# Performance work log

Measured on AMD Instinct MI355X. Metric: run time of the kernel, lower is better.

The kernel has to match this reference:

```python
import jax, jax.numpy as jnp
import numpy as np

HID, INTER, DK = 768, 1536, 128
NEG_INF = 1.0e12
LOG512 = float(np.log(512.0))


def setup_inputs() -> dict:
    key = jax.random.key(0)
    k1, k2, k3 = jax.random.split(key, 3)
    B, S = 4, 2048
    hidden_states = jax.random.normal(k1, (B, S, HID), dtype=jnp.float32)
    attention_mask = jnp.ones((B, S), dtype=jnp.int32)
    # i_dense: hidden -> 2*INTER + DK (no bias); o_dense: INTER -> hidden (no bias)
    Wi = jax.random.normal(k2, (HID, 2 * INTER + DK), dtype=jnp.float32) * (HID ** -0.5)
    Wo = jax.random.normal(k3, (INTER, HID), dtype=jnp.float32) * (INTER ** -0.5)
    q_gamma = jnp.ones((DK,), dtype=jnp.float32)  # ScaleOffset scale, offset=False
    k_gamma = jnp.ones((DK,), dtype=jnp.float32)
    return {"hidden_states": hidden_states, "Wi": Wi, "Wo": Wo,
            "q_gamma": q_gamma, "k_gamma": k_gamma,
            "attention_mask": attention_mask}


def reference(hidden_states, Wi, Wo, q_gamma, k_gamma, attention_mask):
    # i_dense + swish, then split into u, v, qk
    x = jax.nn.silu(jnp.einsum('bsh,ho->bso', hidden_states, Wi))
    u = x[..., :INTER]
    v = x[..., INTER:2 * INTER]
    qk = x[..., 2 * INTER:]
    q = qk * q_gamma
    k = qk * k_gamma
    # single-head attention scores
    a = jnp.einsum('bmd,bnd->bmn', q, k) / (DK ** 0.5)
    mask = attention_mask[:, None, :]  # [B,1,N]
    a = jnp.where(mask == 0, -NEG_INF, a)
    l = jnp.sum(attention_mask, axis=-1, keepdims=True)[:, :, None].astype(a.dtype)  # [B,1,1]
    # softmax_plus: softmax(a * log(l) / log(512))
    A = jax.nn.softmax(a * jnp.log(l) / LOG512, axis=-1)
    # dropout inactive in eval mode
    o = jnp.einsum('bmi,ih->bmh', u * jnp.einsum('bmn,bnd->bmd', A, v), Wo)
    return o
```

## Files before the change

### kernel.cpp

```cpp
#include <hip/hip_runtime.h>
#include <hip/hip_bf16.h>
#include <math.h>

#define BATCH 4
#define SEQ   2048
#define HID   768
#define INTER 1536
#define DK    128
#define NTOT  3200
#define MROWS 8192
#define LN512 6.2383246250395075f

typedef _Float16 half8   __attribute__((ext_vector_type(8)));
typedef float    floatx4 __attribute__((ext_vector_type(4)));
typedef float    floatx16 __attribute__((ext_vector_type(16)));

typedef const __attribute__((address_space(1))) unsigned int* gas1_t;
typedef __attribute__((address_space(3))) unsigned int* las3_t;

static __device__ __forceinline__ void load16(const _Float16* g, _Float16* l) {
    __builtin_amdgcn_global_load_lds((gas1_t)g, (las3_t)l, 16, 0, 0);
}
#define WAIT_VM(N)    asm volatile("s_waitcnt vmcnt(" #N ")" ::: "memory")
#define WAIT_LGKM0()  asm volatile("s_waitcnt lgkmcnt(0)" ::: "memory")
#define BARRIER_RAW() asm volatile("s_barrier" ::: "memory")

__global__ void cast_h_kernel(const float* __restrict__ in, _Float16* __restrict__ out, int n) {
    int i = (blockIdx.x * blockDim.x + threadIdx.x) * 8;
    if (i < n) {
        float4 a = *reinterpret_cast<const float4*>(in + i);
        float4 b = *reinterpret_cast<const float4*>(in + i + 4);
        half8 h = {(_Float16)a.x, (_Float16)a.y, (_Float16)a.z, (_Float16)a.w,
                   (_Float16)b.x, (_Float16)b.y, (_Float16)b.z, (_Float16)b.w};
        *reinterpret_cast<half8*>(out + i) = h;
    }
}

__global__ void trans_wi_kernel(const float* __restrict__ Wi, _Float16* __restrict__ WiT) {
    __shared__ _Float16 tile[32][33];
    const int c0 = blockIdx.x * 32, r0 = blockIdx.y * 32;
    const int tx = threadIdx.x, ty = threadIdx.y;
#pragma unroll
    for (int j = 0; j < 32; j += 8)
        tile[tx][ty + j] = (_Float16)Wi[(size_t)(r0 + ty + j) * NTOT + c0 + tx];
    __syncthreads();
#pragma unroll
    for (int j = 0; j < 32; j += 8)
        WiT[(size_t)(c0 + ty + j) * HID + r0 + tx] = tile[ty + j][tx];
}

__global__ void trans_wo_kernel(const float* __restrict__ Wo, _Float16* __restrict__ WoT) {
    __shared__ _Float16 tile[32][33];
    const int c0 = blockIdx.x * 32, r0 = blockIdx.y * 32;
    const int tx = threadIdx.x, ty = threadIdx.y;
#pragma unroll
    for (int j = 0; j < 32; j += 8)
        tile[tx][ty + j] = (_Float16)Wo[(size_t)(r0 + ty + j) * HID + c0 + tx];
    __syncthreads();
#pragma unroll
    for (int j = 0; j < 32; j += 8)
        WoT[(size_t)(c0 + ty + j) * INTER + r0 + tx] = tile[ty + j][tx];
}

__global__ void mask_scales_kernel(const int* __restrict__ mask, float* __restrict__ scales) {
    __shared__ int sh[256];
    int b = blockIdx.x;
    int s = 0;
    for (int i = threadIdx.x; i < SEQ; i += 256) s += mask[b * SEQ + i];
    sh[threadIdx.x] = s;
    __syncthreads();
    for (int off = 128; off > 0; off >>= 1) {
        if (threadIdx.x < off) sh[threadIdx.x] += sh[threadIdx.x + off];
        __syncthreads();
    }
    if (threadIdx.x == 0) scales[b] = logf((float)sh[0]) / LN512;
}

struct TileCtx {
    int tid, wave, lane, quad, l16, l31, half, wm, wn, c0, c1;
};
static __device__ __forceinline__ TileCtx make_ctx() {
    TileCtx t;
    t.tid = threadIdx.x;
    t.wave = t.tid >> 6; t.lane = t.tid & 63;
    t.quad = t.lane >> 4; t.l16 = t.lane & 15;
    t.l31 = t.lane & 31;  t.half = t.lane >> 5;
    t.wm = (t.wave & 1) * 64;
    t.wn = (t.wave >> 1) * 64;
    t.c0 = t.tid;
    t.c1 = t.tid + 256;
    return t;
}

static __device__ __forceinline__ void gemm_mainloop_3s16(
    const TileCtx& t,
    const _Float16* __restrict__ Ag, int lda,
    const _Float16* __restrict__ Bg, int ldb,
    int K, _Float16* smem, floatx4 acc[4][4])
{
    const int ar0 = t.c0 >> 2, ak0 = ((t.c0 & 3) ^ ((t.c0 >> 3) & 3)) * 8;
    const int ar1 = t.c1 >> 2, ak1 = ((t.c1 & 3) ^ ((t.c1 >> 3) & 3)) * 8;
    const _Float16* a0 = Ag + (size_t)ar0 * lda + ak0;
    const _Float16* a1 = Ag + (size_t)ar1 * lda + ak1;
    const _Float16* b0 = Bg + (size_t)ar0 * ldb + ak0;
    const _Float16* b1 = Bg + (size_t)ar1 * ldb + ak1;
    _Float16* Asl = smem + t.c0 * 8;
    _Float16* Bsl = smem + 12288 + t.c0 * 8;
    const int nIter = K >> 5;
    const int sw = (t.l16 >> 1) & 3;
    const int qsw = (t.quad ^ sw) * 8;

    load16(a0, Asl);        load16(a1, Asl + 2048);
    load16(b0, Bsl);        load16(b1, Bsl + 2048);
    if (nIter > 1) {
        load16(a0 + 32, Asl + 4096); load16(a1 + 32, Asl + 6144);
        load16(b0 + 32, Bsl + 4096); load16(b1 + 32, Bsl + 6144);
    }

    int sc = 0, sp = 2;
    for (int k = 0; k < nIter; ++k) {
        if (k + 1 < nIter) { WAIT_VM(4); } else { WAIT_VM(0); }
        BARRIER_RAW();
        if (k + 2 < nIter) {
            const int off = sp * 4096;
            const int k0 = (k + 2) << 5;
            load16(a0 + k0, Asl + off); load16(a1 + k0, Asl + off + 2048);
            load16(b0 + k0, Bsl + off); load16(b1 + k0, Bsl + off + 2048);
        }
        const _Float16* Ab = smem + sc * 4096;
        const _Float16* Bb = smem + 12288 + sc * 4096;
        half8 af[4], bf[4];
#pragma unroll
        for (int mt = 0; mt < 4; ++mt)
            af[mt] = *reinterpret_cast<const half8*>(Ab + (t.wm + mt * 16 + t.l16) * 32 + qsw);
#pragma unroll
        for (int nt = 0; nt < 4; ++nt)
            bf[nt] = *reinterpret_cast<const half8*>(Bb + (t.wn + nt * 16 + t.l16) * 32 + qsw);
#pragma unroll
        for (int mt = 0; mt < 4; ++mt)
#pragma unroll
            for (int nt = 0; nt < 4; ++nt)
                acc[mt][nt] = __builtin_amdgcn_mfma_f32_16x16x32_f16(af[mt], bf[nt], acc[mt][nt], 0, 0, 0);
        WAIT_LGKM0();
        sc = (sc == 2) ? 0 : sc + 1;
        sp = (sp == 2) ? 0 : sp + 1;
    }
}

static __device__ __forceinline__ void gemm_mainloop_3s32(
    const TileCtx& t,
    const _Float16* __restrict__ Ag, int lda,
    const _Float16* __restrict__ Bg, int ldb,
    int K, _Float16* smem, floatx16 acc[2][2])
{
    const int r0i = t.c0 >> 2, s0 = (((r0i >> 1) ^ (r0i >> 3)) & 3);
    const int r1i = t.c1 >> 2, s1 = (((r1i >> 1) ^ (r1i >> 3)) & 3);
    const int ak0 = ((t.c0 & 3) ^ s0) * 8;
    const int ak1 = ((t.c1 & 3) ^ s1) * 8;
    const _Float16* a0 = Ag + (size_t)r0i * lda + ak0;
    const _Float16* a1 = Ag + (size_t)r1i * lda + ak1;
    const _Float16* b0 = Bg + (size_t)r0i * ldb + ak0;
    const _Float16* b1 = Bg + (size_t)r1i * ldb + ak1;
    _Float16* Asl = smem + t.c0 * 8;
    _Float16* Bsl = smem + 12288 + t.c0 * 8;
    const int nIter = K >> 5;

    const int fsw = ((t.l31 >> 1) ^ (t.l31 >> 3)) & 3;

    load16(a0, Asl);        load16(a1, Asl + 2048);
    load16(b0, Bsl);        load16(b1, Bsl + 2048);
    if (nIter > 1) {
        load16(a0 + 32, Asl + 4096); load16(a1 + 32, Asl + 6144);
        load16(b0 + 32, Bsl + 4096); load16(b1 + 32, Bsl + 6144);
    }

    int sc = 0, sp = 2;
    for (int k = 0; k < nIter; ++k) {
        if (k + 1 < nIter) { WAIT_VM(4); } else { WAIT_VM(0); }
        BARRIER_RAW();
        if (k + 2 < nIter) {
            const int off = sp * 4096;
            const int k0 = (k + 2) << 5;
            load16(a0 + k0, Asl + off); load16(a1 + k0, Asl + off + 2048);
            load16(b0 + k0, Bsl + off); load16(b1 + k0, Bsl + off + 2048);
        }
        const _Float16* Ab = smem + sc * 4096;
        const _Float16* Bb = smem + 12288 + sc * 4096;
        half8 af[2][2], bf[2][2];
#pragma unroll
        for (int mt = 0; mt < 2; ++mt)
#pragma unroll
            for (int h = 0; h < 2; ++h)
                af[mt][h] = *reinterpret_cast<const half8*>(
                    Ab + (t.wm + mt * 32 + t.l31) * 32 + (((h * 2 + t.half) ^ fsw) * 8));
#pragma unroll
        for (int nt = 0; nt < 2; ++nt)
#pragma unroll
            for (int h = 0; h < 2; ++h)
                bf[nt][h] = *reinterpret_cast<const half8*>(
                    Bb + (t.wn + nt * 32 + t.l31) * 32 + (((h * 2 + t.half) ^ fsw) * 8));
#pragma unroll
        for (int h = 0; h < 2; ++h)
#pragma unroll
            for (int mt = 0; mt < 2; ++mt)
#pragma unroll
                for (int nt = 0; nt < 2; ++nt)
                    acc[mt][nt] = __builtin_amdgcn_mfma_f32_32x32x16_f16(af[mt][h], bf[nt][h], acc[mt][nt], 0, 0, 0);
        WAIT_LGKM0();
        sc = (sc == 2) ? 0 : sc + 1;
        sp = (sp == 2) ? 0 : sp + 1;
    }
}

__global__ __launch_bounds__(256) void gemm1_kernel(
    const _Float16* __restrict__ Hb, const _Float16* __restrict__ WiT,
    const float* __restrict__ qg, const float* __restrict__ kg,
    _Float16* __restrict__ u, _Float16* __restrict__ vT,
    _Float16* __restrict__ q, _Float16* __restrict__ k)
{
    __shared__ _Float16 smem[24576];
    TileCtx t = make_ctx();
    const int f = blockIdx.x;
    const int xcd = f & 7, i = f >> 3;
    const int m0 = ((xcd << 3) | (i & 7)) * 128;
    const int n0 = (i >> 3) * 128;

    floatx4 acc[4][4] = {};
    gemm_mainloop_3s16(t, Hb + (size_t)m0 * HID, HID, WiT + (size_t)n0 * HID, HID, HID, smem, acc);

    if (n0 >= INTER && n0 < 2 * INTER) {
        __syncthreads();
        const int bb = m0 >> 11, sloc = m0 & (SEQ - 1), cI = n0 - INTER;
#pragma unroll
        for (int mt = 0; mt < 4; ++mt) {
#pragma unroll
            for (int nt = 0; nt < 4; ++nt) {
                int c = t.wn + nt * 16 + t.l16;
#pragma unroll
                for (int i2 = 0; i2 < 4; ++i2) {
                    int r = t.wm + mt * 16 + t.quad * 4 + i2;
                    float x = acc[mt][nt][i2];
                    float y = x / (1.0f + __expf(-x));
                    smem[c * 128 + (r ^ ((c & 15) << 3))] = (_Float16)y;
                }
            }
        }
        __syncthreads();
#pragma unroll
        for (int p = 0; p < 8; ++p) {
            int chunk = t.tid + p * 256;
            int cl = chunk >> 4, sc = chunk & 15;
            int scs = sc ^ (cl & 15);
            half8 v = *reinterpret_cast<const half8*>(smem + cl * 128 + scs * 8);
            *reinterpret_cast<half8*>(vT + ((size_t)bb * INTER + cI + cl) * SEQ + sloc + sc * 8) = v;
        }
    } else {
#pragma unroll
        for (int mt = 0; mt < 4; ++mt) {
#pragma unroll
            for (int nt = 0; nt < 4; ++nt) {
                int col = n0 + t.wn + nt * 16 + t.l16;
#pragma unroll
                for (int i2 = 0; i2 < 4; ++i2) {
                    int row = m0 + t.wm + mt * 16 + t.quad * 4 + i2;
                    float x = acc[mt][nt][i2];
                    float y = x / (1.0f + __expf(-x));
                    if (n0 < INTER) {
                        u[(size_t)row * INTER + col] = (_Float16)y;
                    } else {
                        int c = col - 2 * INTER;
                        q[(size_t)row * DK + c] = (_Float16)(y * qg[c]);
                        k[(size_t)row * DK + c] = (_Float16)(y * kg[c]);
                    }
                }
            }
        }
    }
}

__global__ __launch_bounds__(256) void scores_kernel(
    const _Float16* __restrict__ q, const _Float16* __restrict__ k,
    const int* __restrict__ mask, const float* __restrict__ scales,
    _Float16* __restrict__ P)
{
    const int f = blockIdx.x;
    const int xcd = f & 7, i = f >> 3;
    const int b = xcd >> 1;
    const int m0 = ((xcd & 1) * 64 + i) * 16;
    const int tid = threadIdx.x;
    const int wave = tid >> 6, lane = tid & 63, quad = lane >> 4, l16 = lane & 15;
    const float scale = scales[b];

    half8 aq[4];
    const _Float16* qrow = q + (b * SEQ + m0 + l16) * DK + quad * 8;
#pragma unroll
    for (int kk = 0; kk < 4; ++kk) aq[kk] = *reinterpret_cast<const half8*>(qrow + kk * 32);

    floatx4 sc[32];
#pragma unroll
    for (int nt = 0; nt < 32; ++nt) {
        int n0 = nt * 64 + wave * 16;
        const _Float16* krow = k + (b * SEQ + n0 + l16) * DK + quad * 8;
        floatx4 acc = {};
#pragma unroll
        for (int kk = 0; kk < 4; ++kk) {
            half8 bq = *reinterpret_cast<const half8*>(krow + kk * 32);
            acc = __builtin_amdgcn_mfma_f32_16x16x32_f16(aq[kk], bq, acc, 0, 0, 0);
        }
        sc[nt] = acc;
    }

    const float rs = 0.08838834764831845f * scale;
    const float mval = -1e12f * scale;
    float rmax[4] = {-3.4e38f, -3.4e38f, -3.4e38f, -3.4e38f};
#pragma unroll
    for (int nt = 0; nt < 32; ++nt) {
        int ncol = nt * 64 + wave * 16 + l16;
        bool mok = mask[b * SEQ + ncol] != 0;
#pragma unroll
        for (int i2 = 0; i2 < 4; ++i2) {
            float s = mok ? sc[nt][i2] * rs : mval;
            sc[nt][i2] = s;
            rmax[i2] = fmaxf(rmax[i2], s);
        }
    }
#pragma unroll
    for (int i2 = 0; i2 < 4; ++i2) {
#pragma unroll
        for (int off = 1; off < 16; off <<= 1)
            rmax[i2] = fmaxf(rmax[i2], __shfl_xor(rmax[i2], off, 64));
    }
    __shared__ float redmax[4][16];
    __shared__ float redsum[4][16];
    if (l16 == 0) {
#pragma unroll
        for (int i2 = 0; i2 < 4; ++i2) redmax[wave][quad * 4 + i2] = rmax[i2];
    }
    __syncthreads();
#pragma unroll
    for (int i2 = 0; i2 < 4; ++i2) {
        int r = quad * 4 + i2;
        rmax[i2] = fmaxf(fmaxf(redmax[0][r], redmax[1][r]), fmaxf(redmax[2][r], redmax[3][r]));
    }
    float rsum[4] = {0.f, 0.f, 0.f, 0.f};
#pragma unroll
    for (int nt = 0; nt < 32; ++nt) {
#pragma unroll
        for (int i2 = 0; i2 < 4; ++i2) {
            float e = __expf(sc[nt][i2] - rmax[i2]);
            sc[nt][i2] = e;
            rsum[i2] += e;
        }
    }
#pragma unroll
    for (int i2 = 0; i2 < 4; ++i2) {
#pragma unroll
        for (int off = 1; off < 16; off <<= 1) rsum[i2] += __shfl_xor(rsum[i2], off, 64);
    }
    if (l16 == 0) {
#pragma unroll
        for (int i2 = 0; i2 < 4; ++i2) redsum[wave][quad * 4 + i2] = rsum[i2];
    }
    __syncthreads();
#pragma unroll
    for (int i2 = 0; i2 < 4; ++i2) {
        int r = quad * 4 + i2;
        float tot = redsum[0][r] + redsum[1][r] + redsum[2][r] + redsum[3][r];
        float inv = 1.0f / tot;
        int row = m0 + r;
        _Float16* Prow = P + ((size_t)b * SEQ + row) * SEQ;
#pragma unroll
        for (int nt = 0; nt < 32; ++nt) {
            int ncol = nt * 64 + wave * 16 + l16;
            Prow[ncol] = (_Float16)(sc[nt][i2] * inv);
        }
    }
}

__global__ __launch_bounds__(256) void pv_kernel(
    const _Float16* __restrict__ P, const _Float16* __restrict__ vT,
    _Float16* __restrict__ u)
{
    __shared__ _Float16 smem[24576];
    TileCtx t = make_ctx();
    const int f = blockIdx.x;
    const int xcd = f & 7, i = f >> 3;
    const int b = i / 24, j = i % 24;
    const int m0 = (xcd * 2 + (j & 1)) * 128;
    const int n0 = (j >> 1) * 128;
    const _Float16* Pb  = P  + (size_t)b * SEQ * SEQ;
    const _Float16* vTb = vT + (size_t)b * INTER * SEQ;

    floatx16 acc[2][2] = {};
    gemm_mainloop_3s32(t, Pb + (size_t)m0 * SEQ, SEQ, vTb + (size_t)n0 * SEQ, SEQ, SEQ, smem, acc);

#pragma unroll
    for (int mt = 0; mt < 2; ++mt) {
#pragma unroll
        for (int nt = 0; nt < 2; ++nt) {
            int col = n0 + t.wn + nt * 32 + t.l31;
#pragma unroll
            for (int reg = 0; reg < 16; ++reg) {
                int row = m0 + t.wm + mt * 32 + (reg & 3) + 8 * (reg >> 2) + 4 * t.half;
                size_t gidx = ((size_t)(b * SEQ + row)) * INTER + col;
                float uv = (float)u[gidx];
                u[gidx] = (_Float16)(acc[mt][nt][reg] * uv);
            }
        }
    }
}

__global__ __launch_bounds__(256) void gemm2_kernel(
    const _Float16* __restrict__ tin, const _Float16* __restrict__ WoT,
    float* __restrict__ out)
{
    __shared__ _Float16 smem[24576];
    TileCtx t = make_ctx();
    const int f = blockIdx.x;
    const int xcd = f & 7, i = f >> 3;
    const int m0 = ((xcd << 3) | (i & 7)) * 128;
    const int n0 = (i >> 3) * 128;

    floatx16 acc[2][2] = {};
    gemm_mainloop_3s32(t, tin + (size_t)m0 * INTER, INTER, WoT + (size_t)n0 * INTER, INTER, INTER, smem, acc);

#pragma unroll
    for (int mt = 0; mt < 2; ++mt) {
#pragma unroll
        for (int nt = 0; nt < 2; ++nt) {
            int col = n0 + t.wn + nt * 32 + t.l31;
#pragma unroll
            for (int reg = 0; reg < 16; ++reg) {
                int row = m0 + t.wm + mt * 32 + (reg & 3) + 8 * (reg >> 2) + 4 * t.half;
                out[(size_t)row * HID + col] = acc[mt][nt][reg];
            }
        }
    }
}

extern "C" void kernel_launch(void* const* d_in, const int* in_sizes, int n_in,
                              void* d_out, int out_size, void* d_ws, size_t ws_size,
                              hipStream_t stream) {
    const float* H    = (const float*)d_in[0];
    const float* Wi   = (const float*)d_in[1];
    const float* Wo   = (const float*)d_in[2];
    const float* qg   = (const float*)d_in[3];
    const float* kg   = (const float*)d_in[4];
    const int*   mask = (const int*)d_in[5];
    float* out = (float*)d_out;

    char* base = (char*)d_ws;
    size_t off = 0;
    auto alloc = [&](size_t bytes) { void* p = base + off; off = (off + bytes + 255) & ~(size_t)255; return p; };
    _Float16* Hb   = (_Float16*)alloc((size_t)MROWS * HID * 2);
    _Float16* WiT  = (_Float16*)alloc((size_t)NTOT * HID * 2);
    _Float16* WoT  = (_Float16*)alloc((size_t)HID * INTER * 2);
    _Float16* u    = (_Float16*)alloc((size_t)MROWS * INTER * 2);
    _Float16* vT   = (_Float16*)alloc((size_t)BATCH * INTER * SEQ * 2);
    _Float16* q    = (_Float16*)alloc((size_t)MROWS * DK * 2);
    _Float16* k    = (_Float16*)alloc((size_t)MROWS * DK * 2);
    _Float16* P    = (_Float16*)alloc((size_t)BATCH * SEQ * SEQ * 2);
    float*    scales = (float*)alloc(4 * sizeof(float));

    {
        int n = MROWS * HID;
        cast_h_kernel<<<n / 8 / 256, 256, 0, stream>>>(H, Hb, n);
        trans_wi_kernel<<<dim3(NTOT / 32, HID / 32), dim3(32, 8), 0, stream>>>(Wi, WiT);
        trans_wo_kernel<<<dim3(HID / 32, INTER / 32), dim3(32, 8), 0, stream>>>(Wo, WoT);
        mask_scales_kernel<<<BATCH, 256, 0, stream>>>(mask, scales);
    }
    gemm1_kernel<<<1600, 256, 0, stream>>>(Hb, WiT, qg, kg, u, vT, q, k);
    scores_kernel<<<512, 256, 0, stream>>>(q, k, mask, scales, P);
    pv_kernel<<<768, 256, 0, stream>>>(P, vT, u);
    gemm2_kernel<<<384, 256, 0, stream>>>(u, WoT, out);
}
```

Measured before the change: 313.3 us.

## Enlarge gemm1 to 256x256 tiles with 512 threads and 4-stage pipeline

Rewrites the first projection GEMM to use 256x256 output tiles with 8 waves, a 4-deep global-to-LDS prefetch ring, split A/B half-steps with barriers, and s_setprio around the MFMA bursts. The Wi transpose is zero-padded to 3328 columns so the N dimension divides evenly into 256-wide tiles, and the qk tile keeps only the first two wave columns. The aim is more data reuse per LDS byte and fewer blocks, giving better MFMA utilisation. In exchange it uses 128KB of LDS per block, limiting occupancy, and 416 blocks leaves some tail imbalance on 256 CUs.

```diff
diff --git a/kernel.cpp b/kernel.cpp
--- a/kernel.cpp
+++ b/kernel.cpp
@@ -8,10 +8,12 @@
 #define INTER 1536
 #define DK    128
 #define NTOT  3200
+#define NTOTP 3328
 #define MROWS 8192
 #define LN512 6.2383246250395075f
 
 typedef _Float16 half8   __attribute__((ext_vector_type(8)));
+typedef _Float16 half4   __attribute__((ext_vector_type(4)));
 typedef float    floatx4 __attribute__((ext_vector_type(4)));
 typedef float    floatx16 __attribute__((ext_vector_type(16)));
 
@@ -42,7 +44,9 @@
     const int tx = threadIdx.x, ty = threadIdx.y;
 #pragma unroll
     for (int j = 0; j < 32; j += 8)
-        tile[tx][ty + j] = (_Float16)Wi[(size_t)(r0 + ty + j) * NTOT + c0 + tx];
+        tile[tx][ty + j] = (c0 + tx < NTOT)
+            ? (_Float16)Wi[(size_t)(r0 + ty + j) * NTOT + c0 + tx]
+            : (_Float16)0.0f;
     __syncthreads();
 #pragma unroll
     for (int j = 0; j < 32; j += 8)
@@ -90,61 +94,6 @@
     t.c0 = t.tid;
     t.c1 = t.tid + 256;
     return t;
-}
-
-static __device__ __forceinline__ void gemm_mainloop_3s16(
-    const TileCtx& t,
-    const _Float16* __restrict__ Ag, int lda,
-    const _Float16* __restrict__ Bg, int ldb,
-    int K, _Float16* smem, floatx4 acc[4][4])
-{
-    const int ar0 = t.c0 >> 2, ak0 = ((t.c0 & 3) ^ ((t.c0 >> 3) & 3)) * 8;
-    const int ar1 = t.c1 >> 2, ak1 = ((t.c1 & 3) ^ ((t.c1 >> 3) & 3)) * 8;
-    const _Float16* a0 = Ag + (size_t)ar0 * lda + ak0;
-    const _Float16* a1 = Ag + (size_t)ar1 * lda + ak1;
-    const _Float16* b0 = Bg + (size_t)ar0 * ldb + ak0;
-    const _Float16* b1 = Bg + (size_t)ar1 * ldb + ak1;
-    _Float16* Asl = smem + t.c0 * 8;
-    _Float16* Bsl = smem + 12288 + t.c0 * 8;
-    const int nIter = K >> 5;
-    const int sw = (t.l16 >> 1) & 3;
-    const int qsw = (t.quad ^ sw) * 8;
-
-    load16(a0, Asl);        load16(a1, Asl + 2048);
-    load16(b0, Bsl);        load16(b1, Bsl + 2048);
-    if (nIter > 1) {
-        load16(a0 + 32, Asl + 4096); load16(a1 + 32, Asl + 6144);
-        load16(b0 + 32, Bsl + 4096); load16(b1 + 32, Bsl + 6144);
-    }
-
-    int sc = 0, sp = 2;
-    for (int k = 0; k < nIter; ++k) {
-        if (k + 1 < nIter) { WAIT_VM(4); } else { WAIT_VM(0); }
-        BARRIER_RAW();
-        if (k + 2 < nIter) {
-            const int off = sp * 4096;
-            const int k0 = (k + 2) << 5;
-            load16(a0 + k0, Asl + off); load16(a1 + k0, Asl + off + 2048);
-            load16(b0 + k0, Bsl + off); load16(b1 + k0, Bsl + off + 2048);
-        }
-        const _Float16* Ab = smem + sc * 4096;
-        const _Float16* Bb = smem + 12288 + sc * 4096;
-        half8 af[4], bf[4];
-#pragma unroll
-        for (int mt = 0; mt < 4; ++mt)
-            af[mt] = *reinterpret_cast<const half8*>(Ab + (t.wm + mt * 16 + t.l16) * 32 + qsw);
-#pragma unroll
-        for (int nt = 0; nt < 4; ++nt)
-            bf[nt] = *reinterpret_cast<const half8*>(Bb + (t.wn + nt * 16 + t.l16) * 32 + qsw);
-#pragma unroll
-        for (int mt = 0; mt < 4; ++mt)
-#pragma unroll
-            for (int nt = 0; nt < 4; ++nt)
-                acc[mt][nt] = __builtin_amdgcn_mfma_f32_16x16x32_f16(af[mt], bf[nt], acc[mt][nt], 0, 0, 0);
-        WAIT_LGKM0();
-        sc = (sc == 2) ? 0 : sc + 1;
-        sp = (sp == 2) ? 0 : sp + 1;
-    }
 }
 
 static __device__ __forceinline__ void gemm_mainloop_3s32(
@@ -212,65 +161,157 @@
     }
 }
 
-__global__ __launch_bounds__(256) void gemm1_kernel(
+__global__ __launch_bounds__(512, 2) void gemm1_kernel(
     const _Float16* __restrict__ Hb, const _Float16* __restrict__ WiT,
     const float* __restrict__ qg, const float* __restrict__ kg,
     _Float16* __restrict__ u, _Float16* __restrict__ vT,
     _Float16* __restrict__ q, _Float16* __restrict__ k)
 {
-    __shared__ _Float16 smem[24576];
-    TileCtx t = make_ctx();
+    __shared__ _Float16 smem[65536];
+    const int tid = threadIdx.x;
+    const int lane = tid & 63, wave = tid >> 6;
+    const int quad = lane >> 4, l16 = lane & 15;
+    const int wm = wave >> 2, wn = wave & 3;
+
     const int f = blockIdx.x;
     const int xcd = f & 7, i = f >> 3;
-    const int m0 = ((xcd << 3) | (i & 7)) * 128;
-    const int n0 = (i >> 3) * 128;
-
-    floatx4 acc[4][4] = {};
-    gemm_mainloop_3s16(t, Hb + (size_t)m0 * HID, HID, WiT + (size_t)n0 * HID, HID, HID, smem, acc);
-
-    if (n0 >= INTER && n0 < 2 * INTER) {
-        __syncthreads();
-        const int bb = m0 >> 11, sloc = m0 & (SEQ - 1), cI = n0 - INTER;
-#pragma unroll
-        for (int mt = 0; mt < 4; ++mt) {
+    const int m0 = (xcd * 4 + (i & 3)) * 256;
+    const int ntile = i >> 2;
+    const int n0 = ntile * 256;
+
+    const _Float16* Ag = Hb  + (size_t)m0 * HID;
+    const _Float16* Bg = WiT + (size_t)n0 * HID;
+
+    const int rA = tid >> 2;
+    const int csw = ((tid & 3) ^ ((rA >> 1) & 3)) * 8;
+    const _Float16* pa0 = Ag + (size_t)rA * HID + csw;
+    const _Float16* pa1 = pa0 + (size_t)128 * HID;
+    const _Float16* pb0 = Bg + (size_t)rA * HID + csw;
+    const _Float16* pb1 = pb0 + (size_t)128 * HID;
+
+    const int sw8 = (l16 >> 1) & 3;
+    const int qs  = (quad ^ sw8) * 8;
+    const int aoff = (wm * 128 + l16) * 32 + qs;
+    const int boff = 8192 + (wn * 64 + l16) * 32 + qs;
+
+    floatx4 acc[8][4] = {};
+
+    const int nKt = HID / 32;
+
+#pragma unroll
+    for (int pt = 0; pt < 3; ++pt) {
+        _Float16* ld = smem + pt * 16384 + tid * 8;
+        const int ko = pt * 32;
+        load16(pa0 + ko, ld);
+        load16(pa1 + ko, ld + 4096);
+        load16(pb0 + ko, ld + 8192);
+        load16(pb1 + ko, ld + 12288);
+    }
+    WAIT_VM(8);
+    BARRIER_RAW();
+
+    for (int t = 0; t < nKt; ++t) {
+        const _Float16* sl = smem + (t & 3) * 16384;
+        _Float16* ld = smem + ((t + 3) & 3) * 16384 + tid * 8;
+        const int ko = (t + 3) * 32;
+        const bool pf = (t + 3) < nKt;
+        half8 bf[4];
+        {
+            half8 af[4];
+#pragma unroll
+            for (int mt = 0; mt < 4; ++mt)
+                af[mt] = *reinterpret_cast<const half8*>(sl + aoff + mt * 512);
+#pragma unroll
+            for (int nt = 0; nt < 4; ++nt)
+                bf[nt] = *reinterpret_cast<const half8*>(sl + boff + nt * 512);
+            if (pf) { load16(pa0 + ko, ld); load16(pa1 + ko, ld + 4096); }
+            BARRIER_RAW();
+            __builtin_amdgcn_s_setprio(1);
+#pragma unroll
+            for (int mt = 0; mt < 4; ++mt)
+#pragma unroll
+                for (int nt = 0; nt < 4; ++nt)
+                    acc[mt][nt] = __builtin_amdgcn_mfma_f32_16x16x32_f16(af[mt], bf[nt], acc[mt][nt], 0, 0, 0);
+            __builtin_amdgcn_s_setprio(0);
+            BARRIER_RAW();
+        }
+        {
+            half8 af[4];
+#pragma unroll
+            for (int mt = 0; mt < 4; ++mt)
+                af[mt] = *reinterpret_cast<const half8*>(sl + aoff + (mt + 4) * 512);
+            if (pf) { load16(pb0 + ko, ld + 8192); load16(pb1 + ko, ld + 12288); }
+            if (t <= nKt - 4)      { WAIT_VM(8); }
+            else if (t == nKt - 3) { WAIT_VM(4); }
+            else if (t == nKt - 2) { WAIT_VM(0); }
+            BARRIER_RAW();
+            __builtin_amdgcn_s_setprio(1);
+#pragma unroll
+            for (int mt = 0; mt < 4; ++mt)
+#pragma unroll
+                for (int nt = 0; nt < 4; ++nt)
+                    acc[mt + 4][nt] = __builtin_amdgcn_mfma_f32_16x16x32_f16(af[mt], bf[nt], acc[mt + 4][nt], 0, 0, 0);
+            __builtin_amdgcn_s_setprio(0);
+            BARRIER_RAW();
+        }
+    }
+    __syncthreads();
+
+    if (ntile < 6) {
+#pragma unroll
+        for (int mt = 0; mt < 8; ++mt) {
 #pragma unroll
             for (int nt = 0; nt < 4; ++nt) {
-                int c = t.wn + nt * 16 + t.l16;
+                const int col = n0 + wn * 64 + nt * 16 + l16;
 #pragma unroll
                 for (int i2 = 0; i2 < 4; ++i2) {
-                    int r = t.wm + mt * 16 + t.quad * 4 + i2;
+                    const int row = m0 + wm * 128 + mt * 16 + quad * 4 + i2;
                     float x = acc[mt][nt][i2];
                     float y = x / (1.0f + __expf(-x));
-                    smem[c * 128 + (r ^ ((c & 15) << 3))] = (_Float16)y;
+                    u[(size_t)row * INTER + col] = (_Float16)y;
                 }
             }
         }
+    } else if (ntile < 12) {
+        const int bb = m0 >> 11, sloc = m0 & (SEQ - 1), cI = n0 - INTER;
+#pragma unroll
+        for (int mt = 0; mt < 8; ++mt) {
+#pragma unroll
+            for (int nt = 0; nt < 4; ++nt) {
+                const int cl  = wn * 64 + nt * 16 + l16;
+                const int rl0 = wm * 128 + mt * 16 + quad * 4;
+                half4 pk;
+#pragma unroll
+                for (int i2 = 0; i2 < 4; ++i2) {
+                    float x = acc[mt][nt][i2];
+                    pk[i2] = (_Float16)(x / (1.0f + __expf(-x)));
+                }
+                *reinterpret_cast<half4*>(smem + cl * 256 + (rl0 ^ ((cl & 31) << 3))) = pk;
+            }
+        }
         __syncthreads();
 #pragma unroll
-        for (int p = 0; p < 8; ++p) {
-            int chunk = t.tid + p * 256;
-            int cl = chunk >> 4, sc = chunk & 15;
-            int scs = sc ^ (cl & 15);
-            half8 v = *reinterpret_cast<const half8*>(smem + cl * 128 + scs * 8);
-            *reinterpret_cast<half8*>(vT + ((size_t)bb * INTER + cI + cl) * SEQ + sloc + sc * 8) = v;
+        for (int p = 0; p < 16; ++p) {
+            const int chunk = p * 512 + tid;
+            const int cl = chunk >> 5, scn = chunk & 31;
+            half8 v = *reinterpret_cast<const half8*>(smem + cl * 256 + ((scn ^ (cl & 31)) << 3));
+            *reinterpret_cast<half8*>(vT + ((size_t)bb * INTER + cI + cl) * SEQ + sloc + scn * 8) = v;
         }
     } else {
-#pragma unroll
-        for (int mt = 0; mt < 4; ++mt) {
-#pragma unroll
-            for (int nt = 0; nt < 4; ++nt) {
-                int col = n0 + t.wn + nt * 16 + t.l16;
-#pragma unroll
-                for (int i2 = 0; i2 < 4; ++i2) {
-                    int row = m0 + t.wm + mt * 16 + t.quad * 4 + i2;
-                    float x = acc[mt][nt][i2];
-                    float y = x / (1.0f + __expf(-x));
-                    if (n0 < INTER) {
-                        u[(size_t)row * INTER + col] = (_Float16)y;
-                    } else {
-                        int c = col - 2 * INTER;
-                        q[(size_t)row * DK + c] = (_Float16)(y * qg[c]);
-                        k[(size_t)row * DK + c] = (_Float16)(y * kg[c]);
+        if (wn < 2) {
+#pragma unroll
+            for (int mt = 0; mt < 8; ++mt) {
+#pragma unroll
+                for (int nt = 0; nt < 4; ++nt) {
+                    const int cq = wn * 64 + nt * 16 + l16;
+                    const float qgv = qg[cq], kgv = kg[cq];
+#pragma unroll
+                    for (int i2 = 0; i2 < 4; ++i2) {
+                        const int row = m0 + wm * 128 + mt * 16 + quad * 4 + i2;
+                        float x = acc[mt][nt][i2];
+                        float y = x / (1.0f + __expf(-x));
+                        q[(size_t)row * DK + cq] = (_Float16)(y * qgv);
+                        k[(size_t)row * DK + cq] = (_Float16)(y * kgv);
                     }
                 }
             }
@@ -453,7 +494,7 @@
     size_t off = 0;
     auto alloc = [&](size_t bytes) { void* p = base + off; off = (off + bytes + 255) & ~(size_t)255; return p; };
     _Float16* Hb   = (_Float16*)alloc((size_t)MROWS * HID * 2);
-    _Float16* WiT  = (_Float16*)alloc((size_t)NTOT * HID * 2);
+    _Float16* WiT  = (_Float16*)alloc((size_t)NTOTP * HID * 2);
     _Float16* WoT  = (_Float16*)alloc((size_t)HID * INTER * 2);
     _Float16* u    = (_Float16*)alloc((size_t)MROWS * INTER * 2);
     _Float16* vT   = (_Float16*)alloc((size_t)BATCH * INTER * SEQ * 2);
@@ -465,11 +506,11 @@
     {
         int n = MROWS * HID;
         cast_h_kernel<<<n / 8 / 256, 256, 0, stream>>>(H, Hb, n);
-        trans_wi_kernel<<<dim3(NTOT / 32, HID / 32), dim3(32, 8), 0, stream>>>(Wi, WiT);
+        trans_wi_kernel<<<dim3(NTOTP / 32, HID / 32), dim3(32, 8), 0, stream>>>(Wi, WiT);
         trans_wo_kernel<<<dim3(HID / 32, INTER / 32), dim3(32, 8), 0, stream>>>(Wo, WoT);
         mask_scales_kernel<<<BATCH, 256, 0, stream>>>(mask, scales);
     }
-    gemm1_kernel<<<1600, 256, 0, stream>>>(Hb, WiT, qg, kg, u, vT, q, k);
+    gemm1_kernel<<<416, 512, 0, stream>>>(Hb, WiT, qg, kg, u, vT, q, k);
     scores_kernel<<<512, 256, 0, stream>>>(q, k, mask, scales, P);
     pv_kernel<<<768, 256, 0, stream>>>(P, vT, u);
     gemm2_kernel<<<384, 256, 0, stream>>>(u, WoT, out);
```

Result: faster. 303.6 us (-3.1%).
